# Kernel optimization log

Hardware: AMD Instinct MI355X
Metric: run time of the kernel (lower is better)

Reference implementation:

```python
import jax, jax.numpy as jnp
import numpy as np

B, S, H, A, O = 512, 64, 1024, 1024, 1024
ATT = 64  # attention logit width (== encoder seq len)


def setup_inputs() -> dict:
    key = jax.random.key(0)
    ks = jax.random.split(key, 14)
    s = lambda *sh: 1.0 / np.sqrt(sh[-1])
    return {
        "encoder_outputs": jax.random.normal(ks[0], (B, S, A), jnp.float32),
        "hidden": jax.random.normal(ks[1], (1, B, H), jnp.float32),
        "max_length": 128,
        # attention: Linear(H+O -> 64)
        "Wa": jax.random.normal(ks[2], (ATT, H + O), jnp.float32) * s(H + O),
        "ba": jnp.zeros((ATT,), jnp.float32),
        # attention_combine: Linear(A+O -> H)
        "Wc": jax.random.normal(ks[3], (H, A + O), jnp.float32) * s(A + O),
        "bc": jnp.zeros((H,), jnp.float32),
        # GRU (1 layer): weight_ih [3H,H], weight_hh [3H,H]
        "W_ih": jax.random.normal(ks[4], (3 * H, H), jnp.float32) * s(H),
        "W_hh": jax.random.normal(ks[5], (3 * H, H), jnp.float32) * s(H),
        "b_ih": jnp.zeros((3 * H,), jnp.float32),
        "b_hh": jnp.zeros((3 * H,), jnp.float32),
        # fc_out: Linear(H -> O)
        "Wo": jax.random.normal(ks[6], (O, H), jnp.float32) * s(H),
        "bo": jnp.zeros((O,), jnp.float32),
    }


def _decode(encoder_outputs, h0, max_length, Wa, ba, Wc, bc, W_ih, W_hh, b_ih, b_hh, Wo, bo):
    Hs = h0.shape[-1]
    dec0 = jnp.zeros((encoder_outputs.shape[0], Wo.shape[0]), encoder_outputs.dtype)

    def step(carry, _):
        dec_in, h = carry  # [B,O], [B,H]
        temp = jnp.concatenate([dec_in, h], axis=1)  # [B, O+H]... matches cat(dec, hidden[-1])
        attn_w = jax.nn.softmax(temp @ Wa.T + ba, axis=1)  # [B,64]
        attn_applied = jnp.einsum("bs,bsd->bd", attn_w, encoder_outputs)  # [B,A]
        gru_in = jax.nn.relu(jnp.concatenate([dec_in, attn_applied], axis=1) @ Wc.T + bc)  # [B,H]
        # single-step PyTorch GRU cell
        gi = gru_in @ W_ih.T + b_ih  # [B,3H]
        gh = h @ W_hh.T + b_hh
        r = jax.nn.sigmoid(gi[:, :Hs] + gh[:, :Hs])
        z = jax.nn.sigmoid(gi[:, Hs:2 * Hs] + gh[:, Hs:2 * Hs])
        n = jnp.tanh(gi[:, 2 * Hs:] + r * gh[:, 2 * Hs:])
        h_new = (1.0 - z) * n + z * h
        out_tok = h_new @ Wo.T + bo  # [B,O]
        return (out_tok, h_new), out_tok

    (_, h_fin), outs = jax.lax.scan(step, (dec0, h0[0]), None, length=max_length)
    output_seq = jnp.transpose(outs, (1, 0, 2))  # [B,T,O]
    return output_seq, h_fin[None]


def reference(encoder_outputs, hidden, max_length, Wa, ba, Wc, bc, W_ih, W_hh, b_ih, b_hh, Wo, bo):
    return _decode(encoder_outputs, hidden, max_length, Wa, ba, Wc, bc, W_ih, W_hh, b_ih, b_hh, Wo, bo)
```

## Files before the change

kernel.cpp:

```cpp
#include <hip/hip_runtime.h>
#include <hip/hip_bf16.h>

#define B 512
#define S 64
#define H 1024
#define O 1024
#define T 128
#define ATT 64

typedef __bf16 bf16;
typedef __bf16 bf16x8 __attribute__((ext_vector_type(8)));
typedef __bf16 bf16x4 __attribute__((ext_vector_type(4)));
typedef float f32x4 __attribute__((ext_vector_type(4)));

static __device__ __forceinline__ float bf2f(bf16 b) {
    unsigned short s = __builtin_bit_cast(unsigned short, b);
    unsigned int u = ((unsigned int)s) << 16;
    return __builtin_bit_cast(float, u);
}
static __device__ __forceinline__ bf16 f2bf(float f) {
    unsigned int u = __builtin_bit_cast(unsigned int, f);
    unsigned int r = (u + 0x7fffu + ((u >> 16) & 1u)) >> 16;
    return __builtin_bit_cast(bf16, (unsigned short)r);
}

template <bool RELU>
__global__ __launch_bounds__(256) void gemm_kernel(
    const bf16* __restrict__ A0, const bf16* __restrict__ A1, int splitK,
    const bf16* __restrict__ W, const float* __restrict__ bias, int K,
    float* __restrict__ Cf, long ldc, bf16* __restrict__ Cbf, int ldcbf) {
    const int tid = threadIdx.x;
    const int wave = tid >> 6, lane = tid & 63;
    const int wm = wave >> 1, wn = wave & 1;
    const int quad = lane >> 4, r = lane & 15;
    const int kq = quad * 8;

    const int m0 = blockIdx.y * 32 + wm * 16 + r;
    const int n0 = blockIdx.x * 64 + wn * 32;

    const int lda0 = splitK, lda1 = K - splitK;
    const bf16* a0row = A0 + (long)m0 * lda0;
    const bf16* a1row = A1 + (long)m0 * lda1;
    const bf16* w0 = W + (long)(n0 + r) * K;
    const bf16* w1 = W + (long)(n0 + 16 + r) * K;

    f32x4 acc0 = {0.f, 0.f, 0.f, 0.f}, acc1 = {0.f, 0.f, 0.f, 0.f};

    for (int k0 = 0; k0 < K; k0 += 32) {
        bf16x8 av;
        if (k0 < splitK)
            av = *(const bf16x8*)(a0row + k0 + kq);
        else
            av = *(const bf16x8*)(a1row + (k0 - splitK) + kq);
        bf16x8 bv0 = *(const bf16x8*)(w0 + k0 + kq);
        bf16x8 bv1 = *(const bf16x8*)(w1 + k0 + kq);
        acc0 = __builtin_amdgcn_mfma_f32_16x16x32_bf16(av, bv0, acc0, 0, 0, 0);
        acc1 = __builtin_amdgcn_mfma_f32_16x16x32_bf16(av, bv1, acc1, 0, 0, 0);
    }

    const int mbase = blockIdx.y * 32 + wm * 16 + quad * 4;
    const int nA = n0 + r, nB = n0 + 16 + r;
    const float biasA = bias[nA], biasB = bias[nB];
#pragma unroll
    for (int reg = 0; reg < 4; ++reg) {
        const int m = mbase + reg;
        float vA = acc0[reg] + biasA;
        float vB = acc1[reg] + biasB;
        if (RELU) { vA = fmaxf(vA, 0.f); vB = fmaxf(vB, 0.f); }
        if (Cf) {
            Cf[(long)m * ldc + nA] = vA;
            Cf[(long)m * ldc + nB] = vB;
        }
        if (Cbf) {
            Cbf[(long)m * ldcbf + nA] = f2bf(vA);
            Cbf[(long)m * ldcbf + nB] = f2bf(vB);
        }
    }
}

__global__ __launch_bounds__(256) void attn_logits_kernel(
    const bf16* __restrict__ dec, const bf16* __restrict__ h,
    const bf16* __restrict__ Wa, const float* __restrict__ ba,
    bf16* __restrict__ attn_w) {
    __shared__ float lg[32][64];
    const int tid = threadIdx.x;
    const int wave = tid >> 6, lane = tid & 63;
    const int wm = wave >> 1, wn = wave & 1;
    const int quad = lane >> 4, r = lane & 15;
    const int kq = quad * 8;

    const int m0 = blockIdx.y * 32 + wm * 16 + r;
    const int n0 = wn * 32;

    const bf16* drow = dec + (long)m0 * H;
    const bf16* hrow = h + (long)m0 * H;
    const bf16* w0 = Wa + (long)(n0 + r) * 2048;
    const bf16* w1 = Wa + (long)(n0 + 16 + r) * 2048;

    f32x4 acc0 = {0.f, 0.f, 0.f, 0.f}, acc1 = {0.f, 0.f, 0.f, 0.f};
    for (int k0 = 0; k0 < 2048; k0 += 32) {
        bf16x8 av;
        if (k0 < 1024)
            av = *(const bf16x8*)(drow + k0 + kq);
        else
            av = *(const bf16x8*)(hrow + (k0 - 1024) + kq);
        bf16x8 bv0 = *(const bf16x8*)(w0 + k0 + kq);
        bf16x8 bv1 = *(const bf16x8*)(w1 + k0 + kq);
        acc0 = __builtin_amdgcn_mfma_f32_16x16x32_bf16(av, bv0, acc0, 0, 0, 0);
        acc1 = __builtin_amdgcn_mfma_f32_16x16x32_bf16(av, bv1, acc1, 0, 0, 0);
    }

    const int mloc = wm * 16 + quad * 4;
#pragma unroll
    for (int reg = 0; reg < 4; ++reg) {
        lg[mloc + reg][n0 + r] = acc0[reg] + ba[n0 + r];
        lg[mloc + reg][n0 + 16 + r] = acc1[reg] + ba[n0 + 16 + r];
    }
    __syncthreads();

    if (tid < 32) {
        const int row = tid;
        float mx = -1e30f;
#pragma unroll
        for (int s = 0; s < 64; ++s) mx = fmaxf(mx, lg[row][s]);
        float sum = 0.f;
#pragma unroll
        for (int s = 0; s < 64; ++s) sum += __expf(lg[row][s] - mx);
        const float inv = 1.f / sum;
        const long gb = (long)(blockIdx.y * 32 + row) * 64;
#pragma unroll
        for (int s = 0; s < 64; ++s)
            attn_w[gb + s] = f2bf(__expf(lg[row][s] - mx) * inv);
    }
}

__global__ __launch_bounds__(256) void attn_apply_kernel(
    const bf16* __restrict__ attn_w, const bf16* __restrict__ enc,
    bf16* __restrict__ attn_out) {
    __shared__ float w[64];
    const int b = blockIdx.x >> 2;
    const int d = ((blockIdx.x & 3) << 8) + threadIdx.x;
    if (threadIdx.x < 64) w[threadIdx.x] = bf2f(attn_w[b * 64 + threadIdx.x]);
    __syncthreads();
    const bf16* e = enc + (long)b * (S * 1024) + d;
    float acc = 0.f;
#pragma unroll 8
    for (int s = 0; s < S; ++s) acc += w[s] * bf2f(e[(long)s * 1024]);
    attn_out[(long)b * 1024 + d] = f2bf(acc);
}

__global__ __launch_bounds__(256) void gru_kernel(
    const bf16* __restrict__ gin, const bf16* __restrict__ hbf,
    const bf16* __restrict__ Wih, const bf16* __restrict__ Whh,
    const float* __restrict__ bih, const float* __restrict__ bhh,
    const float* __restrict__ hold, float* __restrict__ hnew,
    bf16* __restrict__ hnewbf) {
    const int tid = threadIdx.x;
    const int wave = tid >> 6, lane = tid & 63;
    const int wm = wave >> 1, wn = wave & 1;
    const int quad = lane >> 4, r = lane & 15;
    const int kq = quad * 8;

    const int m0 = blockIdx.y * 32 + wm * 16 + r;
    const int n0 = blockIdx.x * 64 + wn * 32;

    const bf16* grow = gin + (long)m0 * H;
    const bf16* hrow = hbf + (long)m0 * H;

    const bf16* wi[3][2];
    const bf16* wh[3][2];
#pragma unroll
    for (int g = 0; g < 3; ++g) {
#pragma unroll
        for (int ni = 0; ni < 2; ++ni) {
            const long row = (long)g * H + n0 + ni * 16 + r;
            wi[g][ni] = Wih + row * H;
            wh[g][ni] = Whh + row * H;
        }
    }

    f32x4 aI[3][2], aH[3][2];
#pragma unroll
    for (int g = 0; g < 3; ++g)
#pragma unroll
        for (int ni = 0; ni < 2; ++ni) {
            aI[g][ni] = (f32x4){0.f, 0.f, 0.f, 0.f};
            aH[g][ni] = (f32x4){0.f, 0.f, 0.f, 0.f};
        }

    for (int k0 = 0; k0 < H; k0 += 32) {
        const int ko = k0 + kq;
        bf16x8 ai = *(const bf16x8*)(grow + ko);
        bf16x8 ah = *(const bf16x8*)(hrow + ko);
#pragma unroll
        for (int g = 0; g < 3; ++g) {
#pragma unroll
            for (int ni = 0; ni < 2; ++ni) {
                bf16x8 bi = *(const bf16x8*)(wi[g][ni] + ko);
                aI[g][ni] = __builtin_amdgcn_mfma_f32_16x16x32_bf16(ai, bi, aI[g][ni], 0, 0, 0);
                bf16x8 bh = *(const bf16x8*)(wh[g][ni] + ko);
                aH[g][ni] = __builtin_amdgcn_mfma_f32_16x16x32_bf16(ah, bh, aH[g][ni], 0, 0, 0);
            }
        }
    }

    const int mbase = blockIdx.y * 32 + wm * 16 + quad * 4;
#pragma unroll
    for (int ni = 0; ni < 2; ++ni) {
        const int j = n0 + ni * 16 + r;
        const float bir = bih[j], biz = bih[j + H], bin = bih[j + 2 * H];
        const float bhr = bhh[j], bhz = bhh[j + H], bhn = bhh[j + 2 * H];
#pragma unroll
        for (int reg = 0; reg < 4; ++reg) {
            const int m = mbase + reg;
            const float gir = aI[0][ni][reg] + bir, ghr = aH[0][ni][reg] + bhr;
            const float giz = aI[1][ni][reg] + biz, ghz = aH[1][ni][reg] + bhz;
            const float ginv = aI[2][ni][reg] + bin, ghn = aH[2][ni][reg] + bhn;
            const float rg = 1.f / (1.f + __expf(-(gir + ghr)));
            const float zg = 1.f / (1.f + __expf(-(giz + ghz)));
            const float ng = tanhf(ginv + rg * ghn);
            const long idx = (long)m * H + j;
            const float hv = hold[idx];
            const float hnv = (1.f - zg) * ng + zg * hv;
            hnew[idx] = hnv;
            hnewbf[idx] = f2bf(hnv);
        }
    }
}

__global__ __launch_bounds__(256) void cast_kernel(
    const float* __restrict__ src, bf16* __restrict__ dst, long n4) {
    long i = (long)blockIdx.x * blockDim.x + threadIdx.x;
    const long stride = (long)gridDim.x * blockDim.x;
    for (; i < n4; i += stride) {
        float4 v = ((const float4*)src)[i];
        bf16x4 o = {f2bf(v.x), f2bf(v.y), f2bf(v.z), f2bf(v.w)};
        *(bf16x4*)(dst + 4 * i) = o;
    }
}

__global__ __launch_bounds__(256) void init_h_kernel(
    const float* __restrict__ h0, float* __restrict__ hfp,
    bf16* __restrict__ hbf, long n4) {
    long i = (long)blockIdx.x * blockDim.x + threadIdx.x;
    const long stride = (long)gridDim.x * blockDim.x;
    for (; i < n4; i += stride) {
        float4 v = ((const float4*)h0)[i];
        ((float4*)hfp)[i] = v;
        bf16x4 o = {f2bf(v.x), f2bf(v.y), f2bf(v.z), f2bf(v.w)};
        *(bf16x4*)(hbf + 4 * i) = o;
    }
}

__global__ __launch_bounds__(256) void copy_f32_kernel(
    const float* __restrict__ src, float* __restrict__ dst, long n4) {
    long i = (long)blockIdx.x * blockDim.x + threadIdx.x;
    const long stride = (long)gridDim.x * blockDim.x;
    for (; i < n4; i += stride) ((float4*)dst)[i] = ((const float4*)src)[i];
}

extern "C" void kernel_launch(void* const* d_in, const int* in_sizes, int n_in,
                              void* d_out, int out_size, void* d_ws, size_t ws_size,
                              hipStream_t stream) {
    const float* enc_f = (const float*)d_in[0];
    const float* hidden = (const float*)d_in[1];
    const float* Wa = (const float*)d_in[3];
    const float* ba = (const float*)d_in[4];
    const float* Wc = (const float*)d_in[5];
    const float* bc = (const float*)d_in[6];
    const float* Wih = (const float*)d_in[7];
    const float* Whh = (const float*)d_in[8];
    const float* bih = (const float*)d_in[9];
    const float* bhh = (const float*)d_in[10];
    const float* Wo = (const float*)d_in[11];
    const float* bo = (const float*)d_in[12];
    float* out = (float*)d_out;

    char* p = (char*)d_ws;
    auto carve = [&](long bytes) {
        char* q = p;
        p += (bytes + 255) & ~255L;
        return q;
    };
    bf16* Wa_bf  = (bf16*)carve((long)ATT * 2048 * 2);
    bf16* Wc_bf  = (bf16*)carve((long)H * 2048 * 2);
    bf16* Wih_bf = (bf16*)carve((long)3 * H * H * 2);
    bf16* Whh_bf = (bf16*)carve((long)3 * H * H * 2);
    bf16* Wo_bf  = (bf16*)carve((long)O * H * 2);
    bf16* enc_bf = (bf16*)carve((long)B * S * 1024 * 2);
    bf16* dec_bf = (bf16*)carve((long)B * O * 2);
    bf16* attn_bf = (bf16*)carve((long)B * 1024 * 2);
    bf16* gru_bf = (bf16*)carve((long)B * H * 2);
    bf16* hbfA = (bf16*)carve((long)B * H * 2);
    bf16* hbfB = (bf16*)carve((long)B * H * 2);
    bf16* attn_w = (bf16*)carve((long)B * 64 * 2);
    float* hfpA = (float*)carve((long)B * H * 4);
    float* hfpB = (float*)carve((long)B * H * 4);

    hipMemsetAsync(dec_bf, 0, (long)B * O * 2, stream);
    auto cast = [&](const float* s, bf16* d, long n) {
        long n4 = n / 4;
        int blocks = (int)((n4 + 255) / 256);
        if (blocks > 4096) blocks = 4096;
        cast_kernel<<<blocks, 256, 0, stream>>>(s, d, n4);
    };
    cast(Wa, Wa_bf, (long)ATT * 2048);
    cast(Wc, Wc_bf, (long)H * 2048);
    cast(Wih, Wih_bf, (long)3 * H * H);
    cast(Whh, Whh_bf, (long)3 * H * H);
    cast(Wo, Wo_bf, (long)O * H);
    cast(enc_f, enc_bf, (long)B * S * 1024);
    init_h_kernel<<<512, 256, 0, stream>>>(hidden, hfpA, hbfA, (long)B * H / 4);

    const dim3 blk(256);
    const dim3 grid_gemm(H / 64, B / 32);
    const dim3 grid_attn(1, B / 32);

    for (int t = 0; t < T; ++t) {
        const bf16* hbf_r = (t & 1) ? hbfB : hbfA;
        bf16* hbf_w = (t & 1) ? hbfA : hbfB;
        const float* hfp_r = (t & 1) ? hfpB : hfpA;
        float* hfp_w = (t & 1) ? hfpA : hfpB;

        attn_logits_kernel<<<grid_attn, blk, 0, stream>>>(dec_bf, hbf_r, Wa_bf, ba, attn_w);
        attn_apply_kernel<<<B * 4, blk, 0, stream>>>(attn_w, enc_bf, attn_bf);
        gemm_kernel<true><<<grid_gemm, blk, 0, stream>>>(
            dec_bf, attn_bf, 1024, Wc_bf, bc, 2048, nullptr, 0, gru_bf, H);
        gru_kernel<<<grid_gemm, blk, 0, stream>>>(
            gru_bf, hbf_r, Wih_bf, Whh_bf, bih, bhh, hfp_r, hfp_w, hbf_w);
        gemm_kernel<false><<<grid_gemm, blk, 0, stream>>>(
            hbf_w, hbf_w, 1024, Wo_bf, bo, 1024,
            out + (long)t * O, (long)T * O, dec_bf, O);
    }

    copy_f32_kernel<<<512, 256, 0, stream>>>(hfpA, out + (long)B * T * O, (long)B * H / 4);
}
```

Measured before the change: 17.28 ms.

## Fold fc_out into attention and combine weights, batch output projection across steps

Uses the fact that dec_in equals h_prev @ Wo^T + bo, so Wo is folded into the attention weights and the combine weights once in a precompute step (Wa_dec·Wo and Wc_dec·Wo plus fused biases). This removes the per-step fc_out GEMM from the serial recurrence. When workspace allows, all hidden states are stored and the output projection runs as one large batched GEMM at the end. The attention-apply kernel is also vectorized with 4-wide nontemporal loads. The trade-off is extra setup GEMMs, a large history buffer, and a different bf16 rounding path for the folded weights.

```diff
diff --git a/kernel.cpp b/kernel.cpp
--- a/kernel.cpp
+++ b/kernel.cpp
@@ -24,10 +24,11 @@
     return __builtin_bit_cast(bf16, (unsigned short)r);
 }
 
-template <bool RELU>
+template <bool RELU, int K, int SPLITK, int KSTART>
 __global__ __launch_bounds__(256) void gemm_kernel(
-    const bf16* __restrict__ A0, const bf16* __restrict__ A1, int splitK,
-    const bf16* __restrict__ W, const float* __restrict__ bias, int K,
+    const bf16* __restrict__ A0, long lda0,
+    const bf16* __restrict__ A1, long lda1,
+    const bf16* __restrict__ W, const float* __restrict__ bias,
     float* __restrict__ Cf, long ldc, bf16* __restrict__ Cbf, int ldcbf) {
     const int tid = threadIdx.x;
     const int wave = tid >> 6, lane = tid & 63;
@@ -38,7 +39,6 @@
     const int m0 = blockIdx.y * 32 + wm * 16 + r;
     const int n0 = blockIdx.x * 64 + wn * 32;
 
-    const int lda0 = splitK, lda1 = K - splitK;
     const bf16* a0row = A0 + (long)m0 * lda0;
     const bf16* a1row = A1 + (long)m0 * lda1;
     const bf16* w0 = W + (long)(n0 + r) * K;
@@ -46,12 +46,12 @@
 
     f32x4 acc0 = {0.f, 0.f, 0.f, 0.f}, acc1 = {0.f, 0.f, 0.f, 0.f};
 
-    for (int k0 = 0; k0 < K; k0 += 32) {
+    for (int k0 = KSTART; k0 < K; k0 += 32) {
         bf16x8 av;
-        if (k0 < splitK)
+        if (k0 < SPLITK)
             av = *(const bf16x8*)(a0row + k0 + kq);
         else
-            av = *(const bf16x8*)(a1row + (k0 - splitK) + kq);
+            av = *(const bf16x8*)(a1row + (k0 - SPLITK) + kq);
         bf16x8 bv0 = *(const bf16x8*)(w0 + k0 + kq);
         bf16x8 bv1 = *(const bf16x8*)(w1 + k0 + kq);
         acc0 = __builtin_amdgcn_mfma_f32_16x16x32_bf16(av, bv0, acc0, 0, 0, 0);
@@ -78,10 +78,48 @@
     }
 }
 
+__global__ __launch_bounds__(256) void fcout_batch_kernel(
+    const bf16* __restrict__ Hh, const bf16* __restrict__ Wo,
+    const float* __restrict__ bo, float* __restrict__ out) {
+    const int tid = threadIdx.x;
+    const int wave = tid >> 6, lane = tid & 63;
+    const int wm = wave >> 1, wn = wave & 1;
+    const int quad = lane >> 4, r = lane & 15;
+    const int kq = quad * 8;
+
+    const int m0 = blockIdx.y * 32 + wm * 16 + r;
+    const int n0 = blockIdx.x * 64 + wn * 32;
+
+    const bf16* arow = Hh + (long)m0 * H;
+    const bf16* w0 = Wo + (long)(n0 + r) * H;
+    const bf16* w1 = Wo + (long)(n0 + 16 + r) * H;
+
+    f32x4 acc0 = {0.f, 0.f, 0.f, 0.f}, acc1 = {0.f, 0.f, 0.f, 0.f};
+    for (int k0 = 0; k0 < H; k0 += 32) {
+        bf16x8 av = *(const bf16x8*)(arow + k0 + kq);
+        bf16x8 bv0 = *(const bf16x8*)(w0 + k0 + kq);
+        bf16x8 bv1 = *(const bf16x8*)(w1 + k0 + kq);
+        acc0 = __builtin_amdgcn_mfma_f32_16x16x32_bf16(av, bv0, acc0, 0, 0, 0);
+        acc1 = __builtin_amdgcn_mfma_f32_16x16x32_bf16(av, bv1, acc1, 0, 0, 0);
+    }
+
+    const int mbase = blockIdx.y * 32 + wm * 16 + quad * 4;
+    const int nA = n0 + r, nB = n0 + 16 + r;
+    const float biasA = bo[nA], biasB = bo[nB];
+#pragma unroll
+    for (int reg = 0; reg < 4; ++reg) {
+        const int m = mbase + reg;
+        const int b = m & (B - 1);
+        const int tt = m >> 9;
+        float* orow = out + (long)b * ((long)T * O) + (long)tt * O;
+        orow[nA] = acc0[reg] + biasA;
+        orow[nB] = acc1[reg] + biasB;
+    }
+}
+
 __global__ __launch_bounds__(256) void attn_logits_kernel(
-    const bf16* __restrict__ dec, const bf16* __restrict__ h,
-    const bf16* __restrict__ Wa, const float* __restrict__ ba,
-    bf16* __restrict__ attn_w) {
+    const bf16* __restrict__ h, const bf16* __restrict__ Wlog,
+    const float* __restrict__ bvec, bf16* __restrict__ attn_w) {
     __shared__ float lg[32][64];
     const int tid = threadIdx.x;
     const int wave = tid >> 6, lane = tid & 63;
@@ -92,18 +130,13 @@
     const int m0 = blockIdx.y * 32 + wm * 16 + r;
     const int n0 = wn * 32;
 
-    const bf16* drow = dec + (long)m0 * H;
     const bf16* hrow = h + (long)m0 * H;
-    const bf16* w0 = Wa + (long)(n0 + r) * 2048;
-    const bf16* w1 = Wa + (long)(n0 + 16 + r) * 2048;
+    const bf16* w0 = Wlog + (long)(n0 + r) * H;
+    const bf16* w1 = Wlog + (long)(n0 + 16 + r) * H;
 
     f32x4 acc0 = {0.f, 0.f, 0.f, 0.f}, acc1 = {0.f, 0.f, 0.f, 0.f};
-    for (int k0 = 0; k0 < 2048; k0 += 32) {
-        bf16x8 av;
-        if (k0 < 1024)
-            av = *(const bf16x8*)(drow + k0 + kq);
-        else
-            av = *(const bf16x8*)(hrow + (k0 - 1024) + kq);
+    for (int k0 = 0; k0 < H; k0 += 32) {
+        bf16x8 av = *(const bf16x8*)(hrow + k0 + kq);
         bf16x8 bv0 = *(const bf16x8*)(w0 + k0 + kq);
         bf16x8 bv1 = *(const bf16x8*)(w1 + k0 + kq);
         acc0 = __builtin_amdgcn_mfma_f32_16x16x32_bf16(av, bv0, acc0, 0, 0, 0);
@@ -113,8 +146,8 @@
     const int mloc = wm * 16 + quad * 4;
 #pragma unroll
     for (int reg = 0; reg < 4; ++reg) {
-        lg[mloc + reg][n0 + r] = acc0[reg] + ba[n0 + r];
-        lg[mloc + reg][n0 + 16 + r] = acc1[reg] + ba[n0 + 16 + r];
+        lg[mloc + reg][n0 + r] = acc0[reg] + bvec[n0 + r];
+        lg[mloc + reg][n0 + 16 + r] = acc1[reg] + bvec[n0 + 16 + r];
     }
     __syncthreads();
 
@@ -138,15 +171,25 @@
     const bf16* __restrict__ attn_w, const bf16* __restrict__ enc,
     bf16* __restrict__ attn_out) {
     __shared__ float w[64];
-    const int b = blockIdx.x >> 2;
-    const int d = ((blockIdx.x & 3) << 8) + threadIdx.x;
-    if (threadIdx.x < 64) w[threadIdx.x] = bf2f(attn_w[b * 64 + threadIdx.x]);
+    const int b = blockIdx.x;
+    const int tid = threadIdx.x;
+    if (tid < 64) w[tid] = bf2f(attn_w[b * 64 + tid]);
     __syncthreads();
-    const bf16* e = enc + (long)b * (S * 1024) + d;
-    float acc = 0.f;
-#pragma unroll 8
-    for (int s = 0; s < S; ++s) acc += w[s] * bf2f(e[(long)s * 1024]);
-    attn_out[(long)b * 1024 + d] = f2bf(acc);
+    const bf16* e = enc + (long)b * (S * 1024) + tid * 4;
+    float a0 = 0.f, a1 = 0.f, a2 = 0.f, a3 = 0.f;
+#pragma unroll 16
+    for (int s = 0; s < S; ++s) {
+        unsigned long long raw =
+            __builtin_nontemporal_load((const unsigned long long*)(e + (long)s * 1024));
+        bf16x4 v = __builtin_bit_cast(bf16x4, raw);
+        const float ws = w[s];
+        a0 += ws * bf2f(v[0]);
+        a1 += ws * bf2f(v[1]);
+        a2 += ws * bf2f(v[2]);
+        a3 += ws * bf2f(v[3]);
+    }
+    bf16x4 o = {f2bf(a0), f2bf(a1), f2bf(a2), f2bf(a3)};
+    *(bf16x4*)(attn_out + (long)b * 1024 + tid * 4) = o;
 }
 
 __global__ __launch_bounds__(256) void gru_kernel(
@@ -228,15 +271,58 @@
     }
 }
 
-__global__ __launch_bounds__(256) void cast_kernel(
-    const float* __restrict__ src, bf16* __restrict__ dst, long n4) {
-    long i = (long)blockIdx.x * blockDim.x + threadIdx.x;
+__global__ __launch_bounds__(256) void cast2d_kernel(
+    const float* __restrict__ src, long ld_src, long soff,
+    bf16* __restrict__ dst, long ld_dst, long doff, long rows, long cols4) {
+    const long total = rows * cols4;
     const long stride = (long)gridDim.x * blockDim.x;
-    for (; i < n4; i += stride) {
-        float4 v = ((const float4*)src)[i];
+    for (long i = (long)blockIdx.x * blockDim.x + threadIdx.x; i < total; i += stride) {
+        const long rr = i / cols4;
+        const long c = (i - rr * cols4) << 2;
+        const float4 v = *(const float4*)(src + rr * ld_src + soff + c);
         bf16x4 o = {f2bf(v.x), f2bf(v.y), f2bf(v.z), f2bf(v.w)};
-        *(bf16x4*)(dst + 4 * i) = o;
-    }
+        *(bf16x4*)(dst + rr * ld_dst + doff + c) = o;
+    }
+}
+
+__global__ __launch_bounds__(256) void transpose_cast_kernel(
+    const float* __restrict__ src, bf16* __restrict__ dst, int n) {
+    __shared__ float tile[32][33];
+    const int tx = threadIdx.x & 31, ty = threadIdx.x >> 5;
+    const int x0 = blockIdx.x * 32, y0 = blockIdx.y * 32;
+#pragma unroll
+    for (int i = 0; i < 32; i += 8)
+        tile[ty + i][tx] = src[(long)(y0 + ty + i) * n + x0 + tx];
+    __syncthreads();
+#pragma unroll
+    for (int i = 0; i < 32; i += 8)
+        dst[(long)(x0 + ty + i) * n + y0 + tx] = f2bf(tile[tx][ty + i]);
+}
+
+__global__ __launch_bounds__(256) void addcast_wlog_kernel(
+    const float* __restrict__ P1, const float* __restrict__ Wa,
+    bf16* __restrict__ Wlog1) {
+    const int i = blockIdx.x * 256 + threadIdx.x;
+    if (i < 64 * 1024) {
+        const int rr = i >> 10, c = i & 1023;
+        Wlog1[i] = f2bf(P1[i] + Wa[(long)rr * 2048 + 1024 + c]);
+    }
+}
+
+__global__ __launch_bounds__(256) void bias_fuse_kernel(
+    const float* __restrict__ W, long ld, const float* __restrict__ v,
+    const float* __restrict__ b_in, float* __restrict__ b_out) {
+    __shared__ float red[256];
+    const int r = blockIdx.x, tid = threadIdx.x;
+    float s = 0.f;
+    for (int j = tid; j < 1024; j += 256) s += W[(long)r * ld + j] * v[j];
+    red[tid] = s;
+    __syncthreads();
+    for (int off = 128; off > 0; off >>= 1) {
+        if (tid < off) red[tid] += red[tid + off];
+        __syncthreads();
+    }
+    if (tid == 0) b_out[r] = b_in[r] + red[0];
 }
 
 __global__ __launch_bounds__(256) void init_h_kernel(
@@ -282,56 +368,112 @@
         p += (bytes + 255) & ~255L;
         return q;
     };
-    bf16* Wa_bf  = (bf16*)carve((long)ATT * 2048 * 2);
-    bf16* Wc_bf  = (bf16*)carve((long)H * 2048 * 2);
+    bf16* Wlog0 = (bf16*)carve((long)64 * 1024 * 2);
+    bf16* Wlog1 = (bf16*)carve((long)64 * 1024 * 2);
+    bf16* Wcomb = (bf16*)carve((long)H * 2048 * 2);
     bf16* Wih_bf = (bf16*)carve((long)3 * H * H * 2);
     bf16* Whh_bf = (bf16*)carve((long)3 * H * H * 2);
-    bf16* Wo_bf  = (bf16*)carve((long)O * H * 2);
+    bf16* Wo_bf = (bf16*)carve((long)O * H * 2);
     bf16* enc_bf = (bf16*)carve((long)B * S * 1024 * 2);
-    bf16* dec_bf = (bf16*)carve((long)B * O * 2);
     bf16* attn_bf = (bf16*)carve((long)B * 1024 * 2);
     bf16* gru_bf = (bf16*)carve((long)B * H * 2);
+    bf16* attn_w = (bf16*)carve((long)B * 64 * 2);
+    bf16* h0bf = (bf16*)carve((long)B * H * 2);
     bf16* hbfA = (bf16*)carve((long)B * H * 2);
     bf16* hbfB = (bf16*)carve((long)B * H * 2);
-    bf16* attn_w = (bf16*)carve((long)B * 64 * 2);
     float* hfpA = (float*)carve((long)B * H * 4);
     float* hfpB = (float*)carve((long)B * H * 4);
-
-    hipMemsetAsync(dec_bf, 0, (long)B * O * 2, stream);
-    auto cast = [&](const float* s, bf16* d, long n) {
-        long n4 = n / 4;
-        int blocks = (int)((n4 + 255) / 256);
-        if (blocks > 4096) blocks = 4096;
-        cast_kernel<<<blocks, 256, 0, stream>>>(s, d, n4);
+    float* blog1 = (float*)carve(64 * 4);
+    float* bc2 = (float*)carve((long)H * 4);
+    float* zeros = (float*)carve(1024 * 4);
+
+    const long persistent = (long)(p - (char*)d_ws);
+    const long histBytes = (long)T * B * H * 2;
+    const bool batched = (ws_size >= (size_t)(persistent + histBytes + 256));
+    bf16* hist = batched ? (bf16*)carve(histBytes) : nullptr;
+    auto slot = [&](int t2) -> bf16* {
+        return batched ? hist + (long)t2 * ((long)B * H)
+                       : ((t2 & 1) ? hbfB : hbfA);
     };
-    cast(Wa, Wa_bf, (long)ATT * 2048);
-    cast(Wc, Wc_bf, (long)H * 2048);
-    cast(Wih, Wih_bf, (long)3 * H * H);
-    cast(Whh, Whh_bf, (long)3 * H * H);
-    cast(Wo, Wo_bf, (long)O * H);
-    cast(enc_f, enc_bf, (long)B * S * 1024);
-    init_h_kernel<<<512, 256, 0, stream>>>(hidden, hfpA, hbfA, (long)B * H / 4);
+
+    {
+        char* sp = (char*)enc_bf;
+        auto scarve = [&](long bytes) {
+            char* q = sp;
+            sp += (bytes + 255) & ~255L;
+            return q;
+        };
+        bf16* Wad = (bf16*)scarve((long)64 * 1024 * 2);
+        bf16* Wcd = (bf16*)scarve((long)H * 1024 * 2);
+        bf16* WoT = (bf16*)scarve((long)H * O * 2);
+        float* P1 = (float*)scarve((long)64 * 1024 * 4);
+        float* P2 = (float*)scarve((long)H * 1024 * 4);
+
+        hipMemsetAsync(zeros, 0, 1024 * 4, stream);
+
+        auto cast2d = [&](const float* src, long lds_, long so, bf16* dst,
+                          long ldd, long doff, long rows, long cols) {
+            long n4 = rows * (cols / 4);
+            int blocks = (int)((n4 + 255) / 256);
+            if (blocks > 4096) blocks = 4096;
+            cast2d_kernel<<<blocks, 256, 0, stream>>>(src, lds_, so, dst, ldd,
+                                                      doff, rows, cols / 4);
+        };
+        cast2d(Wa, 2048, 1024, Wlog0, 1024, 0, 64, 1024);
+        cast2d(Wa, 2048, 0, Wad, 1024, 0, 64, 1024);
+        cast2d(Wc, 2048, 0, Wcd, 1024, 0, 1024, 1024);
+        cast2d(Wc, 2048, 1024, Wcomb, 2048, 1024, 1024, 1024);
+        cast2d(Wih, 1024, 0, Wih_bf, 1024, 0, 3 * H, 1024);
+        cast2d(Whh, 1024, 0, Whh_bf, 1024, 0, 3 * H, 1024);
+        cast2d(Wo, 1024, 0, Wo_bf, 1024, 0, O, 1024);
+        transpose_cast_kernel<<<dim3(32, 32), 256, 0, stream>>>(Wo, WoT, 1024);
+
+        gemm_kernel<false, 1024, 1024, 0><<<dim3(16, 2), 256, 0, stream>>>(
+            Wad, 1024, Wad, 1024, WoT, zeros, P1, 1024, nullptr, 0);
+        gemm_kernel<false, 1024, 1024, 0><<<dim3(16, 32), 256, 0, stream>>>(
+            Wcd, 1024, Wcd, 1024, WoT, zeros, P2, 1024, nullptr, 0);
+
+        addcast_wlog_kernel<<<256, 256, 0, stream>>>(P1, Wa, Wlog1);
+        cast2d(P2, 1024, 0, Wcomb, 2048, 0, 1024, 1024);
+
+        bias_fuse_kernel<<<64, 256, 0, stream>>>(Wa, 2048, bo, ba, blog1);
+        bias_fuse_kernel<<<1024, 256, 0, stream>>>(Wc, 2048, bo, bc, bc2);
+
+        cast2d(enc_f, 1024, 0, enc_bf, 1024, 0, (long)B * S, 1024);
+        init_h_kernel<<<512, 256, 0, stream>>>(hidden, hfpA, h0bf, (long)B * H / 4);
+    }
 
     const dim3 blk(256);
-    const dim3 grid_gemm(H / 64, B / 32);
+    const dim3 grid_nm(H / 64, B / 32);
     const dim3 grid_attn(1, B / 32);
 
     for (int t = 0; t < T; ++t) {
-        const bf16* hbf_r = (t & 1) ? hbfB : hbfA;
-        bf16* hbf_w = (t & 1) ? hbfA : hbfB;
+        const bf16* h_in = (t == 0) ? h0bf : slot(t - 1);
+        bf16* h_out = slot(t);
         const float* hfp_r = (t & 1) ? hfpB : hfpA;
         float* hfp_w = (t & 1) ? hfpA : hfpB;
 
-        attn_logits_kernel<<<grid_attn, blk, 0, stream>>>(dec_bf, hbf_r, Wa_bf, ba, attn_w);
-        attn_apply_kernel<<<B * 4, blk, 0, stream>>>(attn_w, enc_bf, attn_bf);
-        gemm_kernel<true><<<grid_gemm, blk, 0, stream>>>(
-            dec_bf, attn_bf, 1024, Wc_bf, bc, 2048, nullptr, 0, gru_bf, H);
-        gru_kernel<<<grid_gemm, blk, 0, stream>>>(
-            gru_bf, hbf_r, Wih_bf, Whh_bf, bih, bhh, hfp_r, hfp_w, hbf_w);
-        gemm_kernel<false><<<grid_gemm, blk, 0, stream>>>(
-            hbf_w, hbf_w, 1024, Wo_bf, bo, 1024,
-            out + (long)t * O, (long)T * O, dec_bf, O);
-    }
-
-    copy_f32_kernel<<<512, 256, 0, stream>>>(hfpA, out + (long)B * T * O, (long)B * H / 4);
-}
+        attn_logits_kernel<<<grid_attn, blk, 0, stream>>>(
+            h_in, t ? Wlog1 : Wlog0, t ? blog1 : ba, attn_w);
+        attn_apply_kernel<<<B, blk, 0, stream>>>(attn_w, enc_bf, attn_bf);
+        if (t == 0)
+            gemm_kernel<true, 2048, 1024, 1024><<<grid_nm, blk, 0, stream>>>(
+                h_in, 1024, attn_bf, 1024, Wcomb, bc, nullptr, 0, gru_bf, H);
+        else
+            gemm_kernel<true, 2048, 1024, 0><<<grid_nm, blk, 0, stream>>>(
+                h_in, 1024, attn_bf, 1024, Wcomb, bc2, nullptr, 0, gru_bf, H);
+        gru_kernel<<<grid_nm, blk, 0, stream>>>(
+            gru_bf, h_in, Wih_bf, Whh_bf, bih, bhh, hfp_r, hfp_w, h_out);
+        if (!batched)
+            gemm_kernel<false, 1024, 1024, 0><<<grid_nm, blk, 0, stream>>>(
+                h_out, 1024, h_out, 1024, Wo_bf, bo,
+                out + (long)t * O, (long)T * O, nullptr, 0);
+    }
+
+    if (batched)
+        fcout_batch_kernel<<<dim3(16, (T * B) / 32), blk, 0, stream>>>(
+            hist, Wo_bf, bo, out);
+
+    copy_f32_kernel<<<512, 256, 0, stream>>>(hfpA, out + (long)B * T * O,
+                                             (long)B * H / 4);
+}
```

Result: faster. 15.48 ms (-10.4%).
